# Kernel tuning notes

Hardware: AMD Instinct MI355X
Metric: run time of the kernel (lower is better)

## Reference

```python
import jax, jax.numpy as jnp
import numpy as np

VOCAB, BLOCK, C, H, L = 65, 60, 384, 6, 6
HS = C // H  # 64
EPS = 1e-5


def _ln(x, g, b):
    mu = jnp.mean(x, axis=-1, keepdims=True)
    var = jnp.mean(jnp.square(x - mu), axis=-1, keepdims=True)
    return (x - mu) * jax.lax.rsqrt(var + EPS) * g + b


def setup_inputs() -> dict:
    key = jax.random.key(0)
    ks = jax.random.split(key, 16)
    std = 0.02
    B, T = 2048, 60
    inp = {
        'context': jax.random.randint(ks[0], (B, T), 0, VOCAB),
        'tok_emb': std * jax.random.normal(ks[1], (VOCAB, C), jnp.float32),
        'pos_emb': std * jax.random.normal(ks[2], (BLOCK, C), jnp.float32),
        # per-head projections stacked: [L, H, C, HS]
        'wq': std * jax.random.normal(ks[3], (L, H, C, HS), jnp.float32),
        'wk': std * jax.random.normal(ks[4], (L, H, C, HS), jnp.float32),
        'wv': std * jax.random.normal(ks[5], (L, H, C, HS), jnp.float32),
        'wo': std * jax.random.normal(ks[6], (L, C, C), jnp.float32),
        'bo': jnp.zeros((L, C), jnp.float32),
        'ln1_g': jnp.ones((L, C), jnp.float32),
        'ln1_b': jnp.zeros((L, C), jnp.float32),
        'ln2_g': jnp.ones((L, C), jnp.float32),
        'ln2_b': jnp.zeros((L, C), jnp.float32),
        'w1': std * jax.random.normal(ks[7], (L, C, 4 * C), jnp.float32),
        'b1': jnp.zeros((L, 4 * C), jnp.float32),
        'w2': std * jax.random.normal(ks[8], (L, 4 * C, C), jnp.float32),
        'b2': jnp.zeros((L, C), jnp.float32),
        'lnf_g': jnp.ones((C,), jnp.float32),
        'lnf_b': jnp.zeros((C,), jnp.float32),
        'lm_w': std * jax.random.normal(ks[9], (C, VOCAB), jnp.float32),
        'lm_b': jnp.zeros((VOCAB,), jnp.float32),
    }
    return inp


def _forward(context, tok_emb, pos_emb, wq, wk, wv, wo, bo,
             ln1_g, ln1_b, ln2_g, ln2_b, w1, b1, w2, b2,
             lnf_g, lnf_b, lm_w, lm_b):
    B, T = context.shape
    x = tok_emb[context] + pos_emb[:T]  # [B,T,C]
    causal = jnp.tril(jnp.ones((T, T), bool))
    neg_inf = jnp.finfo(x.dtype).min

    def block(x, p):
        (wq_l, wk_l, wv_l, wo_l, bo_l, g1, b1n, g2, b2n, w1_l, bb1, w2_l, bb2) = p
        h = _ln(x, g1, b1n)
        q = jnp.einsum('btc,hcd->bhtd', h, wq_l)
        k = jnp.einsum('btc,hcd->bhtd', h, wk_l)
        v = jnp.einsum('btc,hcd->bhtd', h, wv_l)
        scores = jnp.einsum('bhtd,bhsd->bhts', q, k) * (HS ** -0.5)
        scores = jnp.where(causal, scores, neg_inf)
        probs = jax.nn.softmax(scores, axis=-1)
        o = jnp.einsum('bhts,bhsd->bhtd', probs, v)
        o = o.transpose(0, 2, 1, 3).reshape(B, T, C)  # concat heads
        x = x + o @ wo_l + bo_l
        h = _ln(x, g2, b2n)
        x = x + jax.nn.relu(h @ w1_l + bb1) @ w2_l + bb2
        return x, None

    params = (wq, wk, wv, wo, bo, ln1_g, ln1_b, ln2_g, ln2_b, w1, b1, w2, b2)
    x, _ = jax.lax.scan(block, x, params)
    x = _ln(x, lnf_g, lnf_b)
    return x @ lm_w + lm_b  # [B,T,VOCAB]


def reference(context, tok_emb, pos_emb, wq, wk, wv, wo, bo,
              ln1_g, ln1_b, ln2_g, ln2_b, w1, b1, w2, b2,
              lnf_g, lnf_b, lm_w, lm_b):
    return _forward(context, tok_emb, pos_emb, wq, wk, wv, wo, bo,
                    ln1_g, ln1_b, ln2_g, ln2_b, w1, b1, w2, b2,
                    lnf_g, lnf_b, lm_w, lm_b)
```

## Files before the change

### kernel.cpp

```cpp
#include <hip/hip_runtime.h>


#define B_  2048
#define T_  60
#define C_  384
#define H_  6
#define HS_ 64
#define L_  6
#define FF_ 1536
#define V_  65

typedef unsigned int  u32;
typedef unsigned short u16;
typedef short bf16x8 __attribute__((ext_vector_type(8)));
typedef float f32x4  __attribute__((ext_vector_type(4)));

__device__ __forceinline__ float bf2f(u32 u) {
  return __uint_as_float(u << 16);
}
__device__ __forceinline__ u16 f2bf(float f) {
  u32 u = __float_as_uint(f);
  u = u + 0x7FFFu + ((u >> 16) & 1u);
  return (u16)(u >> 16);
}

__global__ void tconv_k(const float* __restrict__ src, u16* __restrict__ dst,
                        int K, int N, long srcStride, int nH, long sL, long sH)
{
  __shared__ float t[32][33];
  int z = blockIdx.z;
  int l = z / nH, hh = z % nH;
  const float* s = src + (long)z * srcStride;
  u16* d = dst + l * sL + hh * sH;
  int n0 = blockIdx.x * 32, k0 = blockIdx.y * 32;
  for (int yy = threadIdx.y; yy < 32; yy += 8) {
    int k = k0 + yy, n = n0 + threadIdx.x;
    t[yy][threadIdx.x] = (k < K && n < N) ? s[(long)k * N + n] : 0.f;
  }
  __syncthreads();
  for (int yy = threadIdx.y; yy < 32; yy += 8) {
    int n = n0 + yy, k = k0 + threadIdx.x;
    if (n < N && k < K) d[(long)n * K + k] = f2bf(t[threadIdx.x][yy]);
  }
}

__global__ __launch_bounds__(256) void embed_k(const int* __restrict__ ctx,
    const float* __restrict__ tok, const float* __restrict__ pos,
    float* __restrict__ x)
{
  int idx = blockIdx.x * 256 + threadIdx.x;
  int row = idx / (C_ / 4);
  int c   = (idx % (C_ / 4)) * 4;
  int t   = row % T_;
  int tk  = ctx[row];
  float4 a = *(const float4*)(tok + (long)tk * C_ + c);
  float4 p = *(const float4*)(pos + (long)t  * C_ + c);
  float4 o = make_float4(a.x + p.x, a.y + p.y, a.z + p.z, a.w + p.w);
  *(float4*)(x + (long)idx * 4) = o;
}

__global__ __launch_bounds__(256) void ln_k(const float* __restrict__ x,
    const float* __restrict__ g, const float* __restrict__ b,
    u16* __restrict__ h)
{
  int lane = threadIdx.x & 63;
  int wv   = threadIdx.x >> 6;
  long row = (long)blockIdx.x * 4 + wv;
  const float* xr = x + row * C_;
  int c0 = lane * 6;
  float v0[6];
  #pragma unroll
  for (int i = 0; i < 6; i++) v0[i] = xr[c0 + i];
  float s = 0.f, sq = 0.f;
  #pragma unroll
  for (int i = 0; i < 6; i++) { s += v0[i]; sq += v0[i] * v0[i]; }
  #pragma unroll
  for (int off = 32; off > 0; off >>= 1) {
    s  += __shfl_xor(s,  off, 64);
    sq += __shfl_xor(sq, off, 64);
  }
  float mu  = s * (1.f / C_);
  float var = sq * (1.f / C_) - mu * mu;
  float rs  = rsqrtf(var + 1e-5f);
  u16* hr = h + row * C_;
  #pragma unroll
  for (int i = 0; i < 6; i++) {
    float hv = (v0[i] - mu) * rs * g[c0 + i] + b[c0 + i];
    hr[c0 + i] = f2bf(hv);
  }
}

template<int RELU, int RES, int OBF>
__global__ __launch_bounds__(256) void gemm128d(const u16* __restrict__ A,
    const u16* __restrict__ Wt, const float* __restrict__ bias,
    const float* __restrict__ resid, void* __restrict__ outp,
    int N, int K, int mT, int nT)
{
  __shared__ __align__(16) u16 As[2][128][4][8];
  __shared__ __align__(16) u16 Bs[2][128][4][8];
  int tid = threadIdx.x;
  int bid = blockIdx.x;
  int mtile, ntile;
  if ((mT & 7) == 0) {
    int xcd = bid & 7, loc = bid >> 3;
    int q = loc / nT;
    mtile = xcd * (mT >> 3) + q;
    ntile = loc - q * nT;
  } else {
    int q = bid / nT;
    mtile = q;
    ntile = bid - q * nT;
  }
  long mBase = (long)mtile * 128;
  int  nBase = ntile * 128;
  int lane = tid & 63, wv = tid >> 6;
  int l15 = lane & 15, l4 = lane >> 4;
  int wr = wv >> 1, wc = wv & 1;
  int sk = tid & 3, sr = tid >> 2;
  int swW = sk ^ ((sr >> 2) & 3);
  int swR = l4 ^ (l15 >> 2);
  const u16* aP = A + (mBase + sr) * (long)K + sk * 8;
  const u16* bP = Wt + ((long)nBase + sr) * K + sk * 8;
  const long rStep = (long)64 * K;

  f32x4 acc[4][4];
  #pragma unroll
  for (int i = 0; i < 4; i++)
    #pragma unroll
    for (int j = 0; j < 4; j++)
      acc[i][j] = (f32x4){0.f, 0.f, 0.f, 0.f};

  uint4 ar0 = *(const uint4*)aP;
  uint4 ar1 = *(const uint4*)(aP + rStep);
  uint4 br0 = *(const uint4*)bP;
  uint4 br1 = *(const uint4*)(bP + rStep);
  *(uint4*)&As[0][sr][swW][0]      = ar0;
  *(uint4*)&As[0][sr + 64][swW][0] = ar1;
  *(uint4*)&Bs[0][sr][swW][0]      = br0;
  *(uint4*)&Bs[0][sr + 64][swW][0] = br1;
  if (K > 32) {
    ar0 = *(const uint4*)(aP + 32);
    ar1 = *(const uint4*)(aP + rStep + 32);
    br0 = *(const uint4*)(bP + 32);
    br1 = *(const uint4*)(bP + rStep + 32);
  }
  __syncthreads();

  int cur = 0;
  for (int k0 = 0; k0 < K; k0 += 32) {
    bf16x8 af[4], bfr[4];
    #pragma unroll
    for (int i = 0; i < 4; i++)
      af[i] = *(const bf16x8*)&As[cur][wr * 64 + i * 16 + l15][swR][0];
    #pragma unroll
    for (int j = 0; j < 4; j++)
      bfr[j] = *(const bf16x8*)&Bs[cur][wc * 64 + j * 16 + l15][swR][0];
    if (k0 + 32 < K) {
      int nb = cur ^ 1;
      *(uint4*)&As[nb][sr][swW][0]      = ar0;
      *(uint4*)&As[nb][sr + 64][swW][0] = ar1;
      *(uint4*)&Bs[nb][sr][swW][0]      = br0;
      *(uint4*)&Bs[nb][sr + 64][swW][0] = br1;
      if (k0 + 64 < K) {
        ar0 = *(const uint4*)(aP + k0 + 64);
        ar1 = *(const uint4*)(aP + rStep + k0 + 64);
        br0 = *(const uint4*)(bP + k0 + 64);
        br1 = *(const uint4*)(bP + rStep + k0 + 64);
      }
    }
    #pragma unroll
    for (int i = 0; i < 4; i++)
      #pragma unroll
      for (int j = 0; j < 4; j++)
        acc[i][j] = __builtin_amdgcn_mfma_f32_16x16x32_bf16(
            af[i], bfr[j], acc[i][j], 0, 0, 0);
    __syncthreads();
    cur ^= 1;
  }

  #pragma unroll
  for (int i = 0; i < 4; i++) {
    #pragma unroll
    for (int j = 0; j < 4; j++) {
      int n = nBase + wc * 64 + j * 16 + l15;
      float bv = bias ? bias[n] : 0.f;
      #pragma unroll
      for (int r = 0; r < 4; r++) {
        long row = mBase + wr * 64 + i * 16 + l4 * 4 + r;
        float vv = acc[i][j][r] + bv;
        if (RELU) vv = fmaxf(vv, 0.f);
        if (RES)  vv += resid[row * N + n];
        if (OBF) ((u16*)outp)[row * N + n] = f2bf(vv);
        else     ((float*)outp)[row * N + n] = vv;
      }
    }
  }
}

template<int OBF>
__global__ __launch_bounds__(256) void gemm_head(const u16* __restrict__ A,
    const u16* __restrict__ Wt, const float* __restrict__ bias,
    void* __restrict__ outp, int N, int K)
{
  __shared__ __align__(16) u16 As[128][4][8];
  __shared__ __align__(16) u16 Bs[64][4][8];
  int tid  = threadIdx.x;
  int nt   = blockIdx.x;
  int nBase = nt * 64;
  long mBase = (long)blockIdx.y * 128;
  int lane = tid & 63, wv = tid >> 6;
  int l15 = lane & 15, l4 = lane >> 4;
  int sseg = tid & 3;
  int srow = tid >> 2;
  int swW = sseg ^ ((srow >> 2) & 3);
  int swR = l4 ^ (l15 >> 2);
  const u16* a0p = A + (mBase + srow) * K + sseg * 8;
  const u16* a1p = a0p + (long)64 * K;
  bool colOK = (nBase + srow) < N;
  const u16* bp  = Wt + (long)(nBase + srow) * K + sseg * 8;

  f32x4 acc[2][4];
  #pragma unroll
  for (int i = 0; i < 2; i++)
    #pragma unroll
    for (int j = 0; j < 4; j++)
      acc[i][j] = (f32x4){0.f, 0.f, 0.f, 0.f};

  for (int k0 = 0; k0 < K; k0 += 32) {
    uint4 av0 = *(const uint4*)(a0p + k0);
    uint4 av1 = *(const uint4*)(a1p + k0);
    uint4 bv  = colOK ? *(const uint4*)(bp + k0) : make_uint4(0, 0, 0, 0);
    *(uint4*)&As[srow][swW][0]      = av0;
    *(uint4*)&As[srow + 64][swW][0] = av1;
    *(uint4*)&Bs[srow][swW][0]      = bv;
    __syncthreads();
    bf16x8 af[2], bfr[4];
    af[0] = *(const bf16x8*)&As[wv * 32 + l15][swR][0];
    af[1] = *(const bf16x8*)&As[wv * 32 + 16 + l15][swR][0];
    #pragma unroll
    for (int j = 0; j < 4; j++)
      bfr[j] = *(const bf16x8*)&Bs[j * 16 + l15][swR][0];
    #pragma unroll
    for (int i = 0; i < 2; i++)
      #pragma unroll
      for (int j = 0; j < 4; j++)
        acc[i][j] = __builtin_amdgcn_mfma_f32_16x16x32_bf16(
            af[i], bfr[j], acc[i][j], 0, 0, 0);
    __syncthreads();
  }

  #pragma unroll
  for (int i = 0; i < 2; i++) {
    #pragma unroll
    for (int j = 0; j < 4; j++) {
      int n = nBase + j * 16 + l15;
      if (n < N) {
        #pragma unroll
        for (int r = 0; r < 4; r++) {
          long row = mBase + wv * 32 + i * 16 + l4 * 4 + r;
          float vv = acc[i][j][r];
          if (bias) vv += bias[n];
          if (OBF) ((u16*)outp)[row * N + n] = f2bf(vv);
          else     ((float*)outp)[row * N + n] = vv;
        }
      }
    }
  }
}

__global__ __launch_bounds__(256) void attn_k(const u16* __restrict__ qkv,
    u16* __restrict__ ao)
{
  __shared__ __align__(16) u16 qs[64][72];
  __shared__ __align__(16) u16 ks[64][72];
  __shared__ __align__(16) u16 vT[64][72];
  __shared__ __align__(16) u16 ps[64][72];
  int tid = threadIdx.x;
  int bb = blockIdx.x / H_;
  int hh = blockIdx.x % H_;
  const u16* base = qkv + ((long)bb * T_) * 1152 + hh * HS_;

  for (int i = tid; i < 576; i += 256)
    ((uint4*)vT)[i] = make_uint4(0, 0, 0, 0);
  __syncthreads();

  for (int i = tid; i < 480; i += 256) {
    int t = i >> 3, d0 = (i & 7) << 3;
    const u16* rp = base + (long)t * 1152;
    *(uint4*)&qs[t][d0] = *(const uint4*)(rp + d0);
    *(uint4*)&ks[t][d0] = *(const uint4*)(rp + 384 + d0);
    uint4 rv = *(const uint4*)(rp + 768 + d0);
    u16 vv[8] = {(u16)(rv.x & 0xffffu), (u16)(rv.x >> 16),
                 (u16)(rv.y & 0xffffu), (u16)(rv.y >> 16),
                 (u16)(rv.z & 0xffffu), (u16)(rv.z >> 16),
                 (u16)(rv.w & 0xffffu), (u16)(rv.w >> 16)};
    #pragma unroll
    for (int m = 0; m < 8; m++) vT[d0 + m][t] = vv[m];
  }
  __syncthreads();

  int lane = tid & 63, wv = tid >> 6;
  int l15 = lane & 15, quad = lane >> 4;

  bf16x8 aq0 = *(const bf16x8*)&qs[wv * 16 + l15][quad * 8];
  bf16x8 aq1 = *(const bf16x8*)&qs[wv * 16 + l15][32 + quad * 8];
  f32x4 s[4];
  #pragma unroll
  for (int jt = 0; jt < 4; jt++) {
    bf16x8 b0 = *(const bf16x8*)&ks[jt * 16 + l15][quad * 8];
    bf16x8 b1 = *(const bf16x8*)&ks[jt * 16 + l15][32 + quad * 8];
    f32x4 a2 = (f32x4){0.f, 0.f, 0.f, 0.f};
    a2 = __builtin_amdgcn_mfma_f32_16x16x32_bf16(aq0, b0, a2, 0, 0, 0);
    a2 = __builtin_amdgcn_mfma_f32_16x16x32_bf16(aq1, b1, a2, 0, 0, 0);
    s[jt] = a2;
  }

  int rbase = wv * 16 + quad * 4;
  #pragma unroll
  for (int r = 0; r < 4; r++) {
    int row = rbase + r;
    float v0[4];
    #pragma unroll
    for (int jt = 0; jt < 4; jt++) {
      int col = jt * 16 + l15;
      float sv = s[jt][r] * 0.125f;
      v0[jt] = (col <= row) ? sv : -1e30f;
    }
    float m = fmaxf(fmaxf(v0[0], v0[1]), fmaxf(v0[2], v0[3]));
    #pragma unroll
    for (int off = 1; off < 16; off <<= 1) m = fmaxf(m, __shfl_xor(m, off, 64));
    float sum = 0.f;
    #pragma unroll
    for (int jt = 0; jt < 4; jt++) { v0[jt] = __expf(v0[jt] - m); sum += v0[jt]; }
    #pragma unroll
    for (int off = 1; off < 16; off <<= 1) sum += __shfl_xor(sum, off, 64);
    float inv = 1.f / sum;
    #pragma unroll
    for (int jt = 0; jt < 4; jt++)
      ps[row][jt * 16 + l15] = f2bf(v0[jt] * inv);
  }
  __syncthreads();

  bf16x8 ap0 = *(const bf16x8*)&ps[wv * 16 + l15][quad * 8];
  bf16x8 ap1 = *(const bf16x8*)&ps[wv * 16 + l15][32 + quad * 8];
  long obase = ((long)bb * T_) * C_ + hh * HS_;
  #pragma unroll
  for (int dt = 0; dt < 4; dt++) {
    bf16x8 b0 = *(const bf16x8*)&vT[dt * 16 + l15][quad * 8];
    bf16x8 b1 = *(const bf16x8*)&vT[dt * 16 + l15][32 + quad * 8];
    f32x4 a2 = (f32x4){0.f, 0.f, 0.f, 0.f};
    a2 = __builtin_amdgcn_mfma_f32_16x16x32_bf16(ap0, b0, a2, 0, 0, 0);
    a2 = __builtin_amdgcn_mfma_f32_16x16x32_bf16(ap1, b1, a2, 0, 0, 0);
    #pragma unroll
    for (int r = 0; r < 4; r++) {
      int row = rbase + r;
      if (row < T_)
        ao[obase + (long)row * C_ + dt * 16 + l15] = f2bf(a2[r]);
    }
  }
}

extern "C" void kernel_launch(void* const* d_in, const int* in_sizes, int n_in,
                              void* d_out, int out_size, void* d_ws, size_t ws_size,
                              hipStream_t stream)
{
  const int*   ctx  = (const int*)  d_in[0];
  const float* tok  = (const float*)d_in[1];
  const float* pos  = (const float*)d_in[2];
  const float* wq   = (const float*)d_in[3];
  const float* wk   = (const float*)d_in[4];
  const float* wv   = (const float*)d_in[5];
  const float* wo   = (const float*)d_in[6];
  const float* bo   = (const float*)d_in[7];
  const float* ln1g = (const float*)d_in[8];
  const float* ln1b = (const float*)d_in[9];
  const float* ln2g = (const float*)d_in[10];
  const float* ln2b = (const float*)d_in[11];
  const float* w1   = (const float*)d_in[12];
  const float* b1   = (const float*)d_in[13];
  const float* w2   = (const float*)d_in[14];
  const float* b2   = (const float*)d_in[15];
  const float* lnfg = (const float*)d_in[16];
  const float* lnfb = (const float*)d_in[17];
  const float* lmw  = (const float*)d_in[18];
  const float* lmb  = (const float*)d_in[19];
  float* out = (float*)d_out;

  const long nQKV = (long)L_ * H_ * C_ * HS_;
  const long nWO  = (long)L_ * C_ * C_;
  const long nW1  = (long)L_ * C_ * FF_;
  const long nLM  = (long)C_ * V_;
  u16* wqkvT = (u16*)d_ws;
  u16* woT = wqkvT + 3 * nQKV;
  u16* w1T = woT + nWO;
  u16* w2T = w1T + nW1;
  u16* lmT = w2T + nW1;
  const size_t wbytes = (size_t)(nQKV * 3 + nWO + nW1 * 2 + nLM) * 2;

  int chunkB = 32;
  {
    const int cand[] = {2048, 1024, 512, 256, 128, 64, 32};
    for (int i = 0; i < 7; i++) {
      size_t U = (size_t)cand[i] * T_ * C_ * 2;
      if (wbytes + 7 * U <= ws_size) { chunkB = cand[i]; break; }
    }
  }
  const long BTc = (long)chunkB * T_;
  char* wsb = (char*)d_ws + wbytes;
  const size_t U = (size_t)BTc * C_ * 2;
  float* x    = (float*)wsb;
  u16*   h    = (u16*)(wsb + 2 * U);
  char*  reg  = wsb + 3 * U;
  u16* qkvb = (u16*)reg;
  u16* ab   = (u16*)(reg + 3 * U);
  u16* fb   = (u16*)reg;

  {
    dim3 tb(32, 8);
    const long sL = 1152L * 384, sH = 64L * 384, sec = 384L * 384;
    tconv_k<<<dim3(2, 12, L_ * H_), tb, 0, stream>>>(wq, wqkvT,
        C_, HS_, (long)C_ * HS_, H_, sL, sH);
    tconv_k<<<dim3(2, 12, L_ * H_), tb, 0, stream>>>(wk, wqkvT + sec,
        C_, HS_, (long)C_ * HS_, H_, sL, sH);
    tconv_k<<<dim3(2, 12, L_ * H_), tb, 0, stream>>>(wv, wqkvT + 2 * sec,
        C_, HS_, (long)C_ * HS_, H_, sL, sH);
    tconv_k<<<dim3(12, 12, L_), tb, 0, stream>>>(wo, woT,
        C_, C_, (long)C_ * C_, 1, (long)C_ * C_, 0);
    tconv_k<<<dim3(48, 12, L_), tb, 0, stream>>>(w1, w1T,
        C_, FF_, (long)C_ * FF_, 1, (long)C_ * FF_, 0);
    tconv_k<<<dim3(12, 48, L_), tb, 0, stream>>>(w2, w2T,
        FF_, C_, (long)FF_ * C_, 1, (long)FF_ * C_, 0);
    tconv_k<<<dim3(3, 12, 1), tb, 0, stream>>>(lmw, lmT,
        C_, V_, (long)C_ * V_, 1, 0, 0);
  }

  const long qkvL = 1152L * 384;
  const long woL  = (long)C_ * C_;
  const long w1L  = (long)C_ * FF_;
  dim3 blk(256);
  dim3 gEmb((u32)(BTc * C_ / 4 / 256));
  dim3 gLN((u32)(BTc / 4));
  int mT = (int)(BTc / 128);
  dim3 gHd(2, (u32)(BTc / 128));
  dim3 gAt((u32)(chunkB * H_));

  for (int c0 = 0; c0 < B_; c0 += chunkB) {
    const long tok0 = (long)c0 * T_;
    const int* ctxc = ctx + tok0;
    float* outc = out + tok0 * V_;

    embed_k<<<gEmb, blk, 0, stream>>>(ctxc, tok, pos, x);

    for (int l = 0; l < L_; l++) {
      ln_k<<<gLN, blk, 0, stream>>>(x, ln1g + l * C_, ln1b + l * C_, h);
      gemm128d<0,0,1><<<dim3(mT * 9), blk, 0, stream>>>(h, wqkvT + l * qkvL,
          nullptr, nullptr, qkvb, 1152, C_, mT, 9);
      attn_k<<<gAt, blk, 0, stream>>>(qkvb, ab);
      gemm128d<0,1,0><<<dim3(mT * 3), blk, 0, stream>>>(ab, woT + l * woL,
          bo + l * C_, x, x, C_, C_, mT, 3);
      ln_k<<<gLN, blk, 0, stream>>>(x, ln2g + l * C_, ln2b + l * C_, h);
      gemm128d<1,0,1><<<dim3(mT * 12), blk, 0, stream>>>(h, w1T + l * w1L,
          b1 + l * FF_, nullptr, fb, FF_, C_, mT, 12);
      gemm128d<0,1,0><<<dim3(mT * 3), blk, 0, stream>>>(fb, w2T + l * w1L,
          b2 + l * C_, x, x, C_, FF_, mT, 3);
    }

    ln_k<<<gLN, blk, 0, stream>>>(x, lnfg, lnfb, h);
    gemm_head<0><<<gHd, blk, 0, stream>>>(h, lmT, lmb, outc, V_, C_);
  }
}
```

Measured before the change: 5.821 ms.

## Stage GEMM tiles with direct global-to-LDS loads and use 8 waves per tile

The 128x128 bf16 GEMM now fills shared memory with global_load_lds, an asynchronous copy from global memory straight into LDS. This replaces the old path that loaded into registers and then stored to LDS. The block grows from 256 to 512 threads, so each wave computes a 32x64 sub-tile instead of 64x64, which halves the accumulator registers and raises the number of waves in flight. The XOR swizzle moves to the global source address, because each wave's LDS destination is a contiguous block. The aim is to cut register pressure and the VGPR round trip for staging, at the cost of more LDS fragment reads per MFMA and reliance on the barrier to wait for the async loads.

```diff
diff --git a/kernel.cpp b/kernel.cpp
--- a/kernel.cpp
+++ b/kernel.cpp
@@ -22,6 +22,12 @@
   u32 u = __float_as_uint(f);
   u = u + 0x7FFFu + ((u >> 16) & 1u);
   return (u16)(u >> 16);
+}
+
+typedef const __attribute__((address_space(1))) unsigned int gas_u32;
+typedef __attribute__((address_space(3))) unsigned int las_u32;
+__device__ __forceinline__ void gload16(const u16* g, u16* l) {
+  __builtin_amdgcn_global_load_lds((gas_u32*)g, (las_u32*)l, 16, 0, 0);
 }
 
 __global__ void tconv_k(const float* __restrict__ src, u16* __restrict__ dst,
@@ -91,7 +97,7 @@
 }
 
 template<int RELU, int RES, int OBF>
-__global__ __launch_bounds__(256) void gemm128d(const u16* __restrict__ A,
+__global__ __launch_bounds__(512) void gemm128g(const u16* __restrict__ A,
     const u16* __restrict__ Wt, const float* __restrict__ bias,
     const float* __restrict__ resid, void* __restrict__ outp,
     int N, int K, int mT, int nT)
@@ -116,60 +122,42 @@
   int lane = tid & 63, wv = tid >> 6;
   int l15 = lane & 15, l4 = lane >> 4;
   int wr = wv >> 1, wc = wv & 1;
-  int sk = tid & 3, sr = tid >> 2;
-  int swW = sk ^ ((sr >> 2) & 3);
+  int srow = tid >> 2;
+  int seg  = (tid & 3) ^ ((tid >> 4) & 3);
+  const u16* aL = A  + (mBase + srow) * (long)K + seg * 8;
+  const u16* bL = Wt + ((long)nBase + srow) * K + seg * 8;
+  u16* aD0 = &As[0][wv << 4][0][0];
+  u16* bD0 = &Bs[0][wv << 4][0][0];
+  u16* aD1 = &As[1][wv << 4][0][0];
+  u16* bD1 = &Bs[1][wv << 4][0][0];
   int swR = l4 ^ (l15 >> 2);
-  const u16* aP = A + (mBase + sr) * (long)K + sk * 8;
-  const u16* bP = Wt + ((long)nBase + sr) * K + sk * 8;
-  const long rStep = (long)64 * K;
-
-  f32x4 acc[4][4];
-  #pragma unroll
-  for (int i = 0; i < 4; i++)
+
+  f32x4 acc[2][4];
+  #pragma unroll
+  for (int i = 0; i < 2; i++)
     #pragma unroll
     for (int j = 0; j < 4; j++)
       acc[i][j] = (f32x4){0.f, 0.f, 0.f, 0.f};
 
-  uint4 ar0 = *(const uint4*)aP;
-  uint4 ar1 = *(const uint4*)(aP + rStep);
-  uint4 br0 = *(const uint4*)bP;
-  uint4 br1 = *(const uint4*)(bP + rStep);
-  *(uint4*)&As[0][sr][swW][0]      = ar0;
-  *(uint4*)&As[0][sr + 64][swW][0] = ar1;
-  *(uint4*)&Bs[0][sr][swW][0]      = br0;
-  *(uint4*)&Bs[0][sr + 64][swW][0] = br1;
-  if (K > 32) {
-    ar0 = *(const uint4*)(aP + 32);
-    ar1 = *(const uint4*)(aP + rStep + 32);
-    br0 = *(const uint4*)(bP + 32);
-    br1 = *(const uint4*)(bP + rStep + 32);
-  }
+  gload16(aL, aD0);
+  gload16(bL, bD0);
   __syncthreads();
 
   int cur = 0;
   for (int k0 = 0; k0 < K; k0 += 32) {
-    bf16x8 af[4], bfr[4];
-    #pragma unroll
-    for (int i = 0; i < 4; i++)
-      af[i] = *(const bf16x8*)&As[cur][wr * 64 + i * 16 + l15][swR][0];
+    if (k0 + 32 < K) {
+      gload16(aL + k0 + 32, cur ? aD0 : aD1);
+      gload16(bL + k0 + 32, cur ? bD0 : bD1);
+    }
+    bf16x8 af[2], bfr[4];
+    #pragma unroll
+    for (int i = 0; i < 2; i++)
+      af[i] = *(const bf16x8*)&As[cur][wr * 32 + i * 16 + l15][swR][0];
     #pragma unroll
     for (int j = 0; j < 4; j++)
       bfr[j] = *(const bf16x8*)&Bs[cur][wc * 64 + j * 16 + l15][swR][0];
-    if (k0 + 32 < K) {
-      int nb = cur ^ 1;
-      *(uint4*)&As[nb][sr][swW][0]      = ar0;
-      *(uint4*)&As[nb][sr + 64][swW][0] = ar1;
-      *(uint4*)&Bs[nb][sr][swW][0]      = br0;
-      *(uint4*)&Bs[nb][sr + 64][swW][0] = br1;
-      if (k0 + 64 < K) {
-        ar0 = *(const uint4*)(aP + k0 + 64);
-        ar1 = *(const uint4*)(aP + rStep + k0 + 64);
-        br0 = *(const uint4*)(bP + k0 + 64);
-        br1 = *(const uint4*)(bP + rStep + k0 + 64);
-      }
-    }
-    #pragma unroll
-    for (int i = 0; i < 4; i++)
+    #pragma unroll
+    for (int i = 0; i < 2; i++)
       #pragma unroll
       for (int j = 0; j < 4; j++)
         acc[i][j] = __builtin_amdgcn_mfma_f32_16x16x32_bf16(
@@ -179,14 +167,14 @@
   }
 
   #pragma unroll
-  for (int i = 0; i < 4; i++) {
+  for (int i = 0; i < 2; i++) {
     #pragma unroll
     for (int j = 0; j < 4; j++) {
       int n = nBase + wc * 64 + j * 16 + l15;
       float bv = bias ? bias[n] : 0.f;
       #pragma unroll
       for (int r = 0; r < 4; r++) {
-        long row = mBase + wr * 64 + i * 16 + l4 * 4 + r;
+        long row = mBase + wr * 32 + i * 16 + l4 * 4 + r;
         float vv = acc[i][j][r] + bv;
         if (RELU) vv = fmaxf(vv, 0.f);
         if (RES)  vv += resid[row * N + n];
@@ -438,6 +426,7 @@
   const long woL  = (long)C_ * C_;
   const long w1L  = (long)C_ * FF_;
   dim3 blk(256);
+  dim3 blk5(512);
   dim3 gEmb((u32)(BTc * C_ / 4 / 256));
   dim3 gLN((u32)(BTc / 4));
   int mT = (int)(BTc / 128);
@@ -453,15 +442,15 @@
 
     for (int l = 0; l < L_; l++) {
       ln_k<<<gLN, blk, 0, stream>>>(x, ln1g + l * C_, ln1b + l * C_, h);
-      gemm128d<0,0,1><<<dim3(mT * 9), blk, 0, stream>>>(h, wqkvT + l * qkvL,
+      gemm128g<0,0,1><<<dim3(mT * 9), blk5, 0, stream>>>(h, wqkvT + l * qkvL,
           nullptr, nullptr, qkvb, 1152, C_, mT, 9);
       attn_k<<<gAt, blk, 0, stream>>>(qkvb, ab);
-      gemm128d<0,1,0><<<dim3(mT * 3), blk, 0, stream>>>(ab, woT + l * woL,
+      gemm128g<0,1,0><<<dim3(mT * 3), blk5, 0, stream>>>(ab, woT + l * woL,
           bo + l * C_, x, x, C_, C_, mT, 3);
       ln_k<<<gLN, blk, 0, stream>>>(x, ln2g + l * C_, ln2b + l * C_, h);
-      gemm128d<1,0,1><<<dim3(mT * 12), blk, 0, stream>>>(h, w1T + l * w1L,
+      gemm128g<1,0,1><<<dim3(mT * 12), blk5, 0, stream>>>(h, w1T + l * w1L,
           b1 + l * FF_, nullptr, fb, FF_, C_, mT, 12);
-      gemm128d<0,1,0><<<dim3(mT * 3), blk, 0, stream>>>(fb, w2T + l * w1L,
+      gemm128g<0,1,0><<<dim3(mT * 3), blk5, 0, stream>>>(fb, w2T + l * w1L,
           b2 + l * C_, x, x, C_, FF_, mT, 3);
     }
 
```

Result: faster. 5.584 ms (-4.1%).
